# Kernel optimization log

Hardware: AMD Instinct MI355X
Metric: run time of the kernel (lower is better)

The kernel has to match this reference:

```python
import jax, jax.numpy as jnp
import numpy as np


def setup_inputs() -> dict:
    key = jax.random.key(0)
    k1, k2, k3 = jax.random.split(key, 3)
    N, C_in, H, W = 16, 64, 256, 256
    C_out, K = 128, 3
    x = jax.random.normal(k1, (N, C_in, H, W), dtype=jnp.float32)
    # kaiming-ish small init for stability through tanh
    conv_weight = jax.random.normal(k2, (C_out, C_in, K, K), dtype=jnp.float32) * 0.05
    conv_bias = jax.random.normal(k3, (C_out,), dtype=jnp.float32) * 0.05
    return {"x": x, "conv_weight": conv_weight, "conv_bias": conv_bias}


def reference(x, conv_weight, conv_bias):
    # VALID conv, stride 1, NCHW / OIHW (matches the CUDA kernel: H_out = H - K + 1)
    y = jax.lax.conv_general_dilated(
        x, conv_weight,
        window_strides=(1, 1), padding='VALID',
        dimension_numbers=('NCHW', 'OIHW', 'NCHW'))
    y = y + conv_bias[None, :, None, None]
    # fused pattern: double tanh then per-pixel min over output channels (keepdim)
    y = jnp.tanh(jnp.tanh(y))
    out = jnp.min(y, axis=1, keepdims=True)  # (N, 1, H_out, W_out)
    return out
```

## Files before the change

kernel.cpp:

```cpp
#include <hip/hip_runtime.h>
#include <stdint.h>

typedef _Float16 half8 __attribute__((ext_vector_type(8)));
typedef float float4v __attribute__((ext_vector_type(4)));

#define H_IN 256
#define W_IN 256
#define H_OUT 254
#define W_OUT 254
#define T_COLS 68
#define A_ROWS 408
#define A_BYTES (A_ROWS * 128)
#define B_SLAB  8192
#define B_BYTES (3 * B_SLAB)
#define MIN_BYTES (2 * 256 * 4)
#define SMEM_BYTES (A_BYTES + B_BYTES + MIN_BYTES)

__global__ void pack_w_kernel(const float* __restrict__ w, _Float16* __restrict__ Bp3) {
    int idx = blockIdx.x * 256 + threadIdx.x;
    if (idx >= 73728) return;
    int g   = idx >> 12;
    int rem = idx & 4095;
    int co  = rem >> 5;
    int s16 = (rem >> 3) & 3;
    int e   = rem & 7;
    int q   = s16 ^ ((co >> 2) & 3);
    int tap = g >> 1, h = g & 1;
    int cin = h * 32 + q * 8 + e;
    int kh  = tap / 3, kw = tap - kh * 3;
    Bp3[idx] = (_Float16)w[(co * 64 + cin) * 9 + kh * 3 + kw];
}

__device__ __forceinline__ int akey(int row) {
    return (((row & 7) ^ ((row >> 3) & 7)) << 4);
}

__global__ __launch_bounds__(512, 4)
void conv_v8_kernel(const float* __restrict__ x,
                    const _Float16* __restrict__ Bp3,
                    const float* __restrict__ bias,
                    float* __restrict__ out) {
    extern __shared__ __align__(16) char smem[];
    char*  Alds   = smem;
    char*  Blds   = smem + A_BYTES;
    float* minbuf = (float*)(smem + A_BYTES + B_BYTES);

    const int tid  = threadIdx.x;
    const int lane = tid & 63;
    const int wave = tid >> 6;
    const int ow0  = blockIdx.x * 64;
    const int oh0  = blockIdx.y * 4;
    const int nb   = blockIdx.z;
    const int wr   = wave >> 1;
    const int wc   = wave & 1;
    const int q    = lane >> 4;
    const int lr   = lane & 15;

#pragma unroll
    for (int s = 0; s < 2; ++s) {
        const char* src = (const char*)Bp3 + s * B_SLAB + tid * 16;
        char* dstb = Blds + s * B_SLAB + (tid & ~63) * 16;
        __builtin_amdgcn_global_load_lds(
            (const __attribute__((address_space(1))) uint32_t*)src,
            (__attribute__((address_space(3))) uint32_t*)dstb, 16, 0, 0);
    }

    float bv[4];
#pragma unroll
    for (int n = 0; n < 4; ++n) bv[n] = bias[wc * 64 + n * 16 + lr];

    {
        const float* xb = x + (size_t)nb * (64 * H_IN * W_IN);
#pragma unroll
        for (int k = 0; k < 2; ++k) {
            int id = tid + 512 * k;
            if (id < 816) {
                int oct  = (unsigned)id / 102u;
                int pxq  = id - oct * 102;
                int row0 = pxq * 4;
                int r    = (unsigned)row0 / (unsigned)T_COLS;
                int c    = row0 - r * T_COLS;
                int ih   = oh0 + r; if (ih > H_IN - 1) ih = H_IN - 1;
                int iw   = ow0 + c; if (iw > W_IN - 4) iw = W_IN - 4;
                const float* src = xb + (size_t)(oct * 8) * (H_IN * W_IN)
                                      + (size_t)ih * W_IN + iw;
                float4v f[8];
#pragma unroll
                for (int u = 0; u < 8; ++u)
                    f[u] = *(const float4v*)(src + (size_t)u * (H_IN * W_IN));
#pragma unroll
                for (int j = 0; j < 4; ++j) {
                    int row = row0 + j;
                    half8 hv;
#pragma unroll
                    for (int u = 0; u < 8; ++u) hv[u] = (_Float16)f[u][j];
                    *(half8*)(Alds + row * 128 + ((oct * 16) ^ akey(row))) = hv;
                }
            }
        }
    }
    __syncthreads();

    float4v acc[4][4];
#pragma unroll
    for (int m = 0; m < 4; ++m)
#pragma unroll
        for (int n = 0; n < 4; ++n)
#pragma unroll
            for (int i = 0; i < 4; ++i) acc[m][n][i] = 0.0f;

    const int bslot = (q ^ ((lr >> 2) & 3)) << 4;
    const int bco   = (wc * 64 + lr) * 64;

#pragma unroll
    for (int g = 0; g < 18; ++g) {
        if (g < 17) asm volatile("s_waitcnt vmcnt(1)" ::: "memory");
        else        asm volatile("s_waitcnt vmcnt(0)" ::: "memory");
        __builtin_amdgcn_s_barrier();
        __builtin_amdgcn_sched_barrier(0);

        if (g < 16) {
            const char* src = (const char*)Bp3 + (size_t)(g + 2) * B_SLAB + tid * 16;
            char* dstb = Blds + ((g + 2) % 3) * B_SLAB + (tid & ~63) * 16;
            __builtin_amdgcn_global_load_lds(
                (const __attribute__((address_space(1))) uint32_t*)src,
                (__attribute__((address_space(3))) uint32_t*)dstb, 16, 0, 0);
        }

        const int tap = g >> 1, h = g & 1;
        const int kh = tap / 3, kw = tap - kh * 3;
        const int kb = h * 64 + q * 16;

        half8 a[4], b[4];
#pragma unroll
        for (int n = 0; n < 4; ++n)
            b[n] = *(const half8*)(Blds + (g % 3) * B_SLAB + bco + n * 1024 + bslot);
#pragma unroll
        for (int m = 0; m < 4; ++m) {
            int row = (wr + kh) * T_COLS + m * 16 + lr + kw;
            a[m] = *(const half8*)(Alds + row * 128 + (kb ^ akey(row)));
        }

        __builtin_amdgcn_s_setprio(1);
#pragma unroll
        for (int m = 0; m < 4; ++m)
#pragma unroll
            for (int n = 0; n < 4; ++n)
                acc[m][n] = __builtin_amdgcn_mfma_f32_16x16x32_f16(
                    a[m], b[n], acc[m][n], 0, 0, 0);
        __builtin_amdgcn_s_setprio(0);
    }

#pragma unroll
    for (int m = 0; m < 4; ++m) {
        float4v v;
#pragma unroll
        for (int n = 0; n < 4; ++n) {
#pragma unroll
            for (int i = 0; i < 4; ++i) {
                float t = acc[m][n][i] + bv[n];
                v[i] = (n == 0) ? t : fminf(v[i], t);
            }
        }
#pragma unroll
        for (int off = 1; off < 16; off <<= 1)
#pragma unroll
            for (int i = 0; i < 4; ++i)
                v[i] = fminf(v[i], __shfl_xor(v[i], off, 64));
        if (lr == 0) {
#pragma unroll
            for (int i = 0; i < 4; ++i)
                minbuf[wc * 256 + wr * 64 + m * 16 + q * 4 + i] = v[i];
        }
    }
    __syncthreads();

    if (tid < 256) {
        int r = tid >> 6, c = tid & 63;
        int oh = oh0 + r, ow = ow0 + c;
        if (oh < H_OUT && ow < W_OUT) {
            float mv = fminf(minbuf[tid], minbuf[256 + tid]);
            out[((size_t)nb * H_OUT + oh) * W_OUT + ow] = tanhf(tanhf(mv));
        }
    }
}

extern "C" void kernel_launch(void* const* d_in, const int* in_sizes, int n_in,
                              void* d_out, int out_size, void* d_ws, size_t ws_size,
                              hipStream_t stream) {
    const float* x    = (const float*)d_in[0];
    const float* w    = (const float*)d_in[1];
    const float* bias = (const float*)d_in[2];
    float* out        = (float*)d_out;
    _Float16* Bp3     = (_Float16*)d_ws;

    pack_w_kernel<<<dim3(288), dim3(256), 0, stream>>>(w, Bp3);
    conv_v8_kernel<<<dim3(4, 64, 16), dim3(512), SMEM_BYTES, stream>>>(x, Bp3, bias, out);
}
```

Before: 168.6 us.

## Halve block to 4 waves with 8x4 MFMA tiles and register double-buffered LDS fragments

Each block now runs 256 threads (4 waves) instead of 512, and each wave computes 8x4 MFMA tiles covering two output rows. A and B fragments are prefetched from LDS into registers one k-step ahead, and B slabs are loaded three ahead with two loads per thread. The aim is more MFMA work per LDS fragment load and overlap of LDS reads with compute. The cost is a much larger accumulator register footprint (128 floats plus double-buffered fragments), which limits occupancy. The input staging loop also takes more iterations per thread.

```diff
diff --git a/kernel.cpp b/kernel.cpp
--- a/kernel.cpp
+++ b/kernel.cpp
@@ -35,8 +35,8 @@
     return (((row & 7) ^ ((row >> 3) & 7)) << 4);
 }
 
-__global__ __launch_bounds__(512, 4)
-void conv_v8_kernel(const float* __restrict__ x,
+__global__ __launch_bounds__(256, 2)
+void conv_v9_kernel(const float* __restrict__ x,
                     const _Float16* __restrict__ Bp3,
                     const float* __restrict__ bias,
                     float* __restrict__ out) {
@@ -57,102 +57,120 @@
     const int lr   = lane & 15;
 
 #pragma unroll
-    for (int s = 0; s < 2; ++s) {
-        const char* src = (const char*)Bp3 + s * B_SLAB + tid * 16;
-        char* dstb = Blds + s * B_SLAB + (tid & ~63) * 16;
-        __builtin_amdgcn_global_load_lds(
-            (const __attribute__((address_space(1))) uint32_t*)src,
-            (__attribute__((address_space(3))) uint32_t*)dstb, 16, 0, 0);
-    }
-
-    float bv[4];
-#pragma unroll
-    for (int n = 0; n < 4; ++n) bv[n] = bias[wc * 64 + n * 16 + lr];
-
-    {
-        const float* xb = x + (size_t)nb * (64 * H_IN * W_IN);
-#pragma unroll
-        for (int k = 0; k < 2; ++k) {
-            int id = tid + 512 * k;
-            if (id < 816) {
-                int oct  = (unsigned)id / 102u;
-                int pxq  = id - oct * 102;
-                int row0 = pxq * 4;
-                int r    = (unsigned)row0 / (unsigned)T_COLS;
-                int c    = row0 - r * T_COLS;
-                int ih   = oh0 + r; if (ih > H_IN - 1) ih = H_IN - 1;
-                int iw   = ow0 + c; if (iw > W_IN - 4) iw = W_IN - 4;
-                const float* src = xb + (size_t)(oct * 8) * (H_IN * W_IN)
-                                      + (size_t)ih * W_IN + iw;
-                float4v f[8];
-#pragma unroll
-                for (int u = 0; u < 8; ++u)
-                    f[u] = *(const float4v*)(src + (size_t)u * (H_IN * W_IN));
-#pragma unroll
-                for (int j = 0; j < 4; ++j) {
-                    int row = row0 + j;
-                    half8 hv;
-#pragma unroll
-                    for (int u = 0; u < 8; ++u) hv[u] = (_Float16)f[u][j];
-                    *(half8*)(Alds + row * 128 + ((oct * 16) ^ akey(row))) = hv;
-                }
-            }
-        }
-    }
-    __syncthreads();
-
-    float4v acc[4][4];
-#pragma unroll
-    for (int m = 0; m < 4; ++m)
-#pragma unroll
-        for (int n = 0; n < 4; ++n)
-#pragma unroll
-            for (int i = 0; i < 4; ++i) acc[m][n][i] = 0.0f;
-
-    const int bslot = (q ^ ((lr >> 2) & 3)) << 4;
-    const int bco   = (wc * 64 + lr) * 64;
-
-#pragma unroll
-    for (int g = 0; g < 18; ++g) {
-        if (g < 17) asm volatile("s_waitcnt vmcnt(1)" ::: "memory");
-        else        asm volatile("s_waitcnt vmcnt(0)" ::: "memory");
-        __builtin_amdgcn_s_barrier();
-        __builtin_amdgcn_sched_barrier(0);
-
-        if (g < 16) {
-            const char* src = (const char*)Bp3 + (size_t)(g + 2) * B_SLAB + tid * 16;
-            char* dstb = Blds + ((g + 2) % 3) * B_SLAB + (tid & ~63) * 16;
+    for (int s = 0; s < 3; ++s) {
+#pragma unroll
+        for (int i = 0; i < 2; ++i) {
+            const char* src = (const char*)Bp3 + s * B_SLAB + i * 4096 + tid * 16;
+            char* dstb = Blds + s * B_SLAB + i * 4096 + (tid & ~63) * 16;
             __builtin_amdgcn_global_load_lds(
                 (const __attribute__((address_space(1))) uint32_t*)src,
                 (__attribute__((address_space(3))) uint32_t*)dstb, 16, 0, 0);
         }
-
-        const int tap = g >> 1, h = g & 1;
+    }
+
+    float bv[4];
+#pragma unroll
+    for (int n = 0; n < 4; ++n) bv[n] = bias[wc * 64 + n * 16 + lr];
+
+    {
+        const float* xb = x + (size_t)nb * (64 * H_IN * W_IN);
+        for (int id = tid; id < 816; id += 256) {
+            int oct  = (unsigned)id / 102u;
+            int pxq  = id - oct * 102;
+            int row0 = pxq * 4;
+            int r    = (unsigned)row0 / (unsigned)T_COLS;
+            int c    = row0 - r * T_COLS;
+            int ih   = oh0 + r; if (ih > H_IN - 1) ih = H_IN - 1;
+            int iw   = ow0 + c; if (iw > W_IN - 4) iw = W_IN - 4;
+            const float* src = xb + (size_t)(oct * 8) * (H_IN * W_IN)
+                                  + (size_t)ih * W_IN + iw;
+            float4v f[8];
+#pragma unroll
+            for (int u = 0; u < 8; ++u)
+                f[u] = *(const float4v*)(src + (size_t)u * (H_IN * W_IN));
+#pragma unroll
+            for (int j = 0; j < 4; ++j) {
+                int row = row0 + j;
+                half8 hv;
+#pragma unroll
+                for (int u = 0; u < 8; ++u) hv[u] = (_Float16)f[u][j];
+                *(half8*)(Alds + row * 128 + ((oct * 16) ^ akey(row))) = hv;
+            }
+        }
+    }
+    __syncthreads();
+
+    const int bslot = (q ^ ((lr >> 2) & 3)) << 4;
+    const int bco   = (wc * 64 + lr) * 64;
+
+    float4v acc[8][4];
+#pragma unroll
+    for (int m = 0; m < 8; ++m)
+#pragma unroll
+        for (int n = 0; n < 4; ++n)
+#pragma unroll
+            for (int i = 0; i < 4; ++i) acc[m][n][i] = 0.0f;
+
+    half8 acur[8], bcur[4], anxt[8], bnxt[4];
+
+    auto loadA = [&](int gg, half8 (&dst)[8]) {
+        const int tap = gg >> 1, hh = gg & 1;
         const int kh = tap / 3, kw = tap - kh * 3;
-        const int kb = h * 64 + q * 16;
-
-        half8 a[4], b[4];
+        const int kb = hh * 64 + q * 16;
+#pragma unroll
+        for (int m = 0; m < 8; ++m) {
+            int row = (wr * 2 + (m >> 2) + kh) * T_COLS + (m & 3) * 16 + lr + kw;
+            dst[m] = *(const half8*)(Alds + row * 128 + (kb ^ akey(row)));
+        }
+    };
+    auto loadB = [&](int gg, half8 (&dst)[4]) {
 #pragma unroll
         for (int n = 0; n < 4; ++n)
-            b[n] = *(const half8*)(Blds + (g % 3) * B_SLAB + bco + n * 1024 + bslot);
-#pragma unroll
-        for (int m = 0; m < 4; ++m) {
-            int row = (wr + kh) * T_COLS + m * 16 + lr + kw;
-            a[m] = *(const half8*)(Alds + row * 128 + (kb ^ akey(row)));
-        }
-
+            dst[n] = *(const half8*)(Blds + (gg % 3) * B_SLAB + bco + n * 1024 + bslot);
+    };
+
+    loadA(0, acur);
+    loadB(0, bcur);
+
+#pragma unroll
+    for (int g = 0; g < 18; ++g) {
+        if (g < 16)      asm volatile("s_waitcnt vmcnt(2)" ::: "memory");
+        else if (g == 16) asm volatile("s_waitcnt vmcnt(0)" ::: "memory");
+        if (g < 17) __builtin_amdgcn_s_barrier();
+
+        if (g < 15) {
+#pragma unroll
+            for (int i = 0; i < 2; ++i) {
+                const char* src = (const char*)Bp3 + (size_t)(g + 3) * B_SLAB
+                                  + i * 4096 + tid * 16;
+                char* dstb = Blds + ((g + 3) % 3) * B_SLAB + i * 4096
+                                  + (tid & ~63) * 16;
+                __builtin_amdgcn_global_load_lds(
+                    (const __attribute__((address_space(1))) uint32_t*)src,
+                    (__attribute__((address_space(3))) uint32_t*)dstb, 16, 0, 0);
+            }
+        }
+
+        if (g < 17) {
+            if (g & 1) { loadA(g + 1, acur); loadB(g + 1, bcur); }
+            else       { loadA(g + 1, anxt); loadB(g + 1, bnxt); }
+            __builtin_amdgcn_sched_group_barrier(0x100, 12, 0);
+        }
+
+        half8 (&A)[8] = (g & 1) ? anxt : acur;
+        half8 (&B)[4] = (g & 1) ? bnxt : bcur;
         __builtin_amdgcn_s_setprio(1);
 #pragma unroll
-        for (int m = 0; m < 4; ++m)
+        for (int m = 0; m < 8; ++m)
 #pragma unroll
             for (int n = 0; n < 4; ++n)
                 acc[m][n] = __builtin_amdgcn_mfma_f32_16x16x32_f16(
-                    a[m], b[n], acc[m][n], 0, 0, 0);
+                    A[m], B[n], acc[m][n], 0, 0, 0);
         __builtin_amdgcn_s_setprio(0);
     }
 
 #pragma unroll
-    for (int m = 0; m < 4; ++m) {
+    for (int m = 0; m < 8; ++m) {
         float4v v;
 #pragma unroll
         for (int n = 0; n < 4; ++n) {
@@ -170,12 +188,12 @@
         if (lr == 0) {
 #pragma unroll
             for (int i = 0; i < 4; ++i)
-                minbuf[wc * 256 + wr * 64 + m * 16 + q * 4 + i] = v[i];
+                minbuf[wc * 256 + wr * 128 + m * 16 + q * 4 + i] = v[i];
         }
     }
     __syncthreads();
 
-    if (tid < 256) {
+    {
         int r = tid >> 6, c = tid & 63;
         int oh = oh0 + r, ow = ow0 + c;
         if (oh < H_OUT && ow < W_OUT) {
@@ -195,5 +213,5 @@
     _Float16* Bp3     = (_Float16*)d_ws;
 
     pack_w_kernel<<<dim3(288), dim3(256), 0, stream>>>(w, Bp3);
-    conv_v8_kernel<<<dim3(4, 64, 16), dim3(512), SMEM_BYTES, stream>>>(x, Bp3, bias, out);
-}
+    conv_v9_kernel<<<dim3(4, 64, 16), dim3(256), SMEM_BYTES, stream>>>(x, Bp3, bias, out);
+}
```

After: 253.4 us. 50.3% more time.

## Deepen weight ring to four slabs and register-double-buffer LDS fragments

Applied to the files above, without the earlier changes.

The weight staging ring in LDS grows from three to four slabs, with a prefetch distance of three, so weights are fetched further ahead of use. The A and B fragments for the next K-step are now read from LDS into a second register set while the current step's MFMAs run, with sched_group_barrier hints to interleave the LDS reads and MFMAs. The goal is to hide LDS read latency and global-to-LDS latency behind matrix math. The cost is more LDS per block and more registers, and launch bounds drop from 4 to 2 blocks per CU, which may reduce occupancy.

```diff
diff --git a/kernel.cpp b/kernel.cpp
--- a/kernel.cpp
+++ b/kernel.cpp
@@ -12,7 +12,7 @@
 #define A_ROWS 408
 #define A_BYTES (A_ROWS * 128)
 #define B_SLAB  8192
-#define B_BYTES (3 * B_SLAB)
+#define B_BYTES (4 * B_SLAB)
 #define MIN_BYTES (2 * 256 * 4)
 #define SMEM_BYTES (A_BYTES + B_BYTES + MIN_BYTES)
 
@@ -35,11 +35,11 @@
     return (((row & 7) ^ ((row >> 3) & 7)) << 4);
 }
 
-__global__ __launch_bounds__(512, 4)
-void conv_v8_kernel(const float* __restrict__ x,
-                    const _Float16* __restrict__ Bp3,
-                    const float* __restrict__ bias,
-                    float* __restrict__ out) {
+__global__ __launch_bounds__(512, 2)
+void conv_v10_kernel(const float* __restrict__ x,
+                     const _Float16* __restrict__ Bp3,
+                     const float* __restrict__ bias,
+                     float* __restrict__ out) {
     extern __shared__ __align__(16) char smem[];
     char*  Alds   = smem;
     char*  Blds   = smem + A_BYTES;
@@ -57,7 +57,7 @@
     const int lr   = lane & 15;
 
 #pragma unroll
-    for (int s = 0; s < 2; ++s) {
+    for (int s = 0; s < 3; ++s) {
         const char* src = (const char*)Bp3 + s * B_SLAB + tid * 16;
         char* dstb = Blds + s * B_SLAB + (tid & ~63) * 16;
         __builtin_amdgcn_global_load_lds(
@@ -101,54 +101,70 @@
     }
     __syncthreads();
 
-    float4v acc[4][4];
-#pragma unroll
-    for (int m = 0; m < 4; ++m)
-#pragma unroll
-        for (int n = 0; n < 4; ++n)
-#pragma unroll
-            for (int i = 0; i < 4; ++i) acc[m][n][i] = 0.0f;
-
     const int bslot = (q ^ ((lr >> 2) & 3)) << 4;
     const int bco   = (wc * 64 + lr) * 64;
 
+    float4v acc[4][4];
+#pragma unroll
+    for (int m = 0; m < 4; ++m)
+#pragma unroll
+        for (int n = 0; n < 4; ++n)
+#pragma unroll
+            for (int i = 0; i < 4; ++i) acc[m][n][i] = 0.0f;
+
+    half8 acur[4], bcur[4], anxt[4], bnxt[4];
+
+    auto loadA = [&](int gg, half8 (&dst)[4]) {
+        const int tap = gg >> 1, hh = gg & 1;
+        const int kh = tap / 3, kw = tap - kh * 3;
+        const int kb = hh * 64 + q * 16;
+#pragma unroll
+        for (int m = 0; m < 4; ++m) {
+            int row = (wr + kh) * T_COLS + m * 16 + lr + kw;
+            dst[m] = *(const half8*)(Alds + row * 128 + (kb ^ akey(row)));
+        }
+    };
+    auto loadB = [&](int gg, half8 (&dst)[4]) {
+#pragma unroll
+        for (int n = 0; n < 4; ++n)
+            dst[n] = *(const half8*)(Blds + (gg & 3) * B_SLAB + bco + n * 1024 + bslot);
+    };
+
+    loadA(0, acur);
+    loadB(0, bcur);
+
 #pragma unroll
     for (int g = 0; g < 18; ++g) {
-        if (g < 17) asm volatile("s_waitcnt vmcnt(1)" ::: "memory");
-        else        asm volatile("s_waitcnt vmcnt(0)" ::: "memory");
-        __builtin_amdgcn_s_barrier();
-        __builtin_amdgcn_sched_barrier(0);
-
-        if (g < 16) {
-            const char* src = (const char*)Bp3 + (size_t)(g + 2) * B_SLAB + tid * 16;
-            char* dstb = Blds + ((g + 2) % 3) * B_SLAB + (tid & ~63) * 16;
+        if (g < 16)       asm volatile("s_waitcnt vmcnt(1)" ::: "memory");
+        else if (g == 16) asm volatile("s_waitcnt vmcnt(0)" ::: "memory");
+        if (g < 16) __builtin_amdgcn_s_barrier();
+
+        if (g < 15) {
+            const char* src = (const char*)Bp3 + (size_t)(g + 3) * B_SLAB + tid * 16;
+            char* dstb = Blds + ((g + 3) & 3) * B_SLAB + (tid & ~63) * 16;
             __builtin_amdgcn_global_load_lds(
                 (const __attribute__((address_space(1))) uint32_t*)src,
                 (__attribute__((address_space(3))) uint32_t*)dstb, 16, 0, 0);
         }
 
-        const int tap = g >> 1, h = g & 1;
-        const int kh = tap / 3, kw = tap - kh * 3;
-        const int kb = h * 64 + q * 16;
-
-        half8 a[4], b[4];
-#pragma unroll
-        for (int n = 0; n < 4; ++n)
-            b[n] = *(const half8*)(Blds + (g % 3) * B_SLAB + bco + n * 1024 + bslot);
-#pragma unroll
-        for (int m = 0; m < 4; ++m) {
-            int row = (wr + kh) * T_COLS + m * 16 + lr + kw;
-            a[m] = *(const half8*)(Alds + row * 128 + (kb ^ akey(row)));
-        }
-
+        if (g < 17) {
+            if (g & 1) { loadA(g + 1, acur); loadB(g + 1, bcur); }
+            else       { loadA(g + 1, anxt); loadB(g + 1, bnxt); }
+        }
+
+        half8 (&A)[4] = (g & 1) ? anxt : acur;
+        half8 (&B)[4] = (g & 1) ? bnxt : bcur;
+
+        __builtin_amdgcn_sched_group_barrier(0x100, 8, 0);
         __builtin_amdgcn_s_setprio(1);
 #pragma unroll
         for (int m = 0; m < 4; ++m)
 #pragma unroll
             for (int n = 0; n < 4; ++n)
                 acc[m][n] = __builtin_amdgcn_mfma_f32_16x16x32_f16(
-                    a[m], b[n], acc[m][n], 0, 0, 0);
+                    A[m], B[n], acc[m][n], 0, 0, 0);
         __builtin_amdgcn_s_setprio(0);
+        __builtin_amdgcn_sched_group_barrier(0x8, 16, 0);
     }
 
 #pragma unroll
@@ -195,5 +211,5 @@
     _Float16* Bp3     = (_Float16*)d_ws;
 
     pack_w_kernel<<<dim3(288), dim3(256), 0, stream>>>(w, Bp3);
-    conv_v8_kernel<<<dim3(4, 64, 16), dim3(512), SMEM_BYTES, stream>>>(x, Bp3, bias, out);
-}
+    conv_v10_kernel<<<dim3(4, 64, 16), dim3(512), SMEM_BYTES, stream>>>(x, Bp3, bias, out);
+}
```

After: 226.5 us. 1.34x slower.

## Make blocks loop over row strips with double-buffered input tiles and per-tap weight slabs

Applied to the files above, without the earlier changes.

Each block now walks 16 consecutive 4-row output tiles of a 64-row strip instead of one tile. The next tile's input is prefetched into registers during the current tile's MMA loop and written into a second LDS buffer. Weights are repacked into one 16KB slab per tap and streamed with double buffering. This amortizes launch and prologue cost and overlaps input loading with compute. In exchange it uses much more LDS, lowering occupancy to about one block per CU, and leaves a small 256-block grid.

```diff
diff --git a/kernel.cpp b/kernel.cpp
--- a/kernel.cpp
+++ b/kernel.cpp
@@ -11,177 +11,205 @@
 #define T_COLS 68
 #define A_ROWS 408
 #define A_BYTES (A_ROWS * 128)
-#define B_SLAB  8192
-#define B_BYTES (3 * B_SLAB)
-#define MIN_BYTES (2 * 256 * 4)
-#define SMEM_BYTES (A_BYTES + B_BYTES + MIN_BYTES)
-
-__global__ void pack_w_kernel(const float* __restrict__ w, _Float16* __restrict__ Bp3) {
+#define B_SLAB  16384
+#define SMEM_BYTES (2*A_BYTES + 2*B_SLAB + 2048)
+
+__global__ void pack_w_kernel(const float* __restrict__ w, _Float16* __restrict__ Bp) {
     int idx = blockIdx.x * 256 + threadIdx.x;
     if (idx >= 73728) return;
-    int g   = idx >> 12;
-    int rem = idx & 4095;
-    int co  = rem >> 5;
-    int s16 = (rem >> 3) & 3;
+    int tap = idx >> 13;
+    int rem = idx & 8191;
+    int co  = rem >> 6;
+    int s   = (rem >> 3) & 7;
     int e   = rem & 7;
-    int q   = s16 ^ ((co >> 2) & 3);
-    int tap = g >> 1, h = g & 1;
+    int hq  = s ^ (co & 7);
+    int h   = hq >> 2, q = hq & 3;
     int cin = h * 32 + q * 8 + e;
     int kh  = tap / 3, kw = tap - kh * 3;
-    Bp3[idx] = (_Float16)w[(co * 64 + cin) * 9 + kh * 3 + kw];
+    Bp[idx] = (_Float16)w[(co * 64 + cin) * 9 + kh * 3 + kw];
 }
 
 __device__ __forceinline__ int akey(int row) {
     return (((row & 7) ^ ((row >> 3) & 7)) << 4);
 }
 
-__global__ __launch_bounds__(512, 4)
-void conv_v8_kernel(const float* __restrict__ x,
-                    const _Float16* __restrict__ Bp3,
-                    const float* __restrict__ bias,
-                    float* __restrict__ out) {
+__global__ __launch_bounds__(512, 2)
+void conv_v11_kernel(const float* __restrict__ x,
+                     const _Float16* __restrict__ Bp,
+                     const float* __restrict__ bias,
+                     float* __restrict__ out) {
     extern __shared__ __align__(16) char smem[];
-    char*  Alds   = smem;
-    char*  Blds   = smem + A_BYTES;
-    float* minbuf = (float*)(smem + A_BYTES + B_BYTES);
+    char*  AldsBase = smem;
+    char*  Blds     = smem + 2 * A_BYTES;
+    float* minbuf   = (float*)(smem + 2 * A_BYTES + 2 * B_SLAB);
 
     const int tid  = threadIdx.x;
     const int lane = tid & 63;
     const int wave = tid >> 6;
     const int ow0  = blockIdx.x * 64;
-    const int oh0  = blockIdx.y * 4;
+    const int strip0 = blockIdx.y * 64;
     const int nb   = blockIdx.z;
     const int wr   = wave >> 1;
     const int wc   = wave & 1;
     const int q    = lane >> 4;
     const int lr   = lane & 15;
 
-#pragma unroll
-    for (int s = 0; s < 2; ++s) {
-        const char* src = (const char*)Bp3 + s * B_SLAB + tid * 16;
-        char* dstb = Blds + s * B_SLAB + (tid & ~63) * 16;
-        __builtin_amdgcn_global_load_lds(
-            (const __attribute__((address_space(1))) uint32_t*)src,
-            (__attribute__((address_space(3))) uint32_t*)dstb, 16, 0, 0);
+    const float* xb = x + (size_t)nb * (64 * H_IN * W_IN);
+
+    int id0 = tid;
+    int id1 = (tid < 304) ? (512 + tid) : tid;
+    const bool w1 = (tid < 304);
+    int  s_oct[2], s_row0[2], s_r[2], s_iw[2];
+    {
+        int ids[2] = {id0, id1};
+#pragma unroll
+        for (int k = 0; k < 2; ++k) {
+            int o   = (unsigned)ids[k] / 102u;
+            int pxq = ids[k] - o * 102;
+            int r   = (unsigned)pxq / 17u;
+            int c4  = (pxq - r * 17) * 4;
+            s_oct[k] = o; s_row0[k] = pxq * 4; s_r[k] = r;
+            int iw = ow0 + c4; if (iw > W_IN - 4) iw = W_IN - 4;
+            s_iw[k] = iw;
+        }
     }
-
-    float bv[4];
-#pragma unroll
-    for (int n = 0; n < 4; ++n) bv[n] = bias[wc * 64 + n * 16 + lr];
-
-    {
-        const float* xb = x + (size_t)nb * (64 * H_IN * W_IN);
+    float4v f[2][8];
+
+    auto issue_loads = [&](int ih0) {
 #pragma unroll
         for (int k = 0; k < 2; ++k) {
-            int id = tid + 512 * k;
-            if (id < 816) {
-                int oct  = (unsigned)id / 102u;
-                int pxq  = id - oct * 102;
-                int row0 = pxq * 4;
-                int r    = (unsigned)row0 / (unsigned)T_COLS;
-                int c    = row0 - r * T_COLS;
-                int ih   = oh0 + r; if (ih > H_IN - 1) ih = H_IN - 1;
-                int iw   = ow0 + c; if (iw > W_IN - 4) iw = W_IN - 4;
-                const float* src = xb + (size_t)(oct * 8) * (H_IN * W_IN)
-                                      + (size_t)ih * W_IN + iw;
-                float4v f[8];
-#pragma unroll
-                for (int u = 0; u < 8; ++u)
-                    f[u] = *(const float4v*)(src + (size_t)u * (H_IN * W_IN));
-#pragma unroll
-                for (int j = 0; j < 4; ++j) {
-                    int row = row0 + j;
-                    half8 hv;
-#pragma unroll
-                    for (int u = 0; u < 8; ++u) hv[u] = (_Float16)f[u][j];
-                    *(half8*)(Alds + row * 128 + ((oct * 16) ^ akey(row))) = hv;
-                }
-            }
-        }
-    }
-    __syncthreads();
-
-    float4v acc[4][4];
-#pragma unroll
-    for (int m = 0; m < 4; ++m)
-#pragma unroll
-        for (int n = 0; n < 4; ++n)
-#pragma unroll
-            for (int i = 0; i < 4; ++i) acc[m][n][i] = 0.0f;
-
-    const int bslot = (q ^ ((lr >> 2) & 3)) << 4;
-    const int bco   = (wc * 64 + lr) * 64;
-
-#pragma unroll
-    for (int g = 0; g < 18; ++g) {
-        if (g < 17) asm volatile("s_waitcnt vmcnt(1)" ::: "memory");
-        else        asm volatile("s_waitcnt vmcnt(0)" ::: "memory");
-        __builtin_amdgcn_s_barrier();
-        __builtin_amdgcn_sched_barrier(0);
-
-        if (g < 16) {
-            const char* src = (const char*)Bp3 + (size_t)(g + 2) * B_SLAB + tid * 16;
-            char* dstb = Blds + ((g + 2) % 3) * B_SLAB + (tid & ~63) * 16;
+            int ih = ih0 + s_r[k]; if (ih > H_IN - 1) ih = H_IN - 1;
+            const float* src = xb + (size_t)(s_oct[k] * 8) * (H_IN * W_IN)
+                                  + (size_t)ih * W_IN + s_iw[k];
+#pragma unroll
+            for (int u = 0; u < 8; ++u)
+                f[k][u] = *(const float4v*)(src + (size_t)u * (H_IN * W_IN));
+        }
+    };
+    auto write_A = [&](char* abuf) {
+#pragma unroll
+        for (int k = 0; k < 2; ++k) {
+            if (k == 1 && !w1) continue;
+#pragma unroll
+            for (int j = 0; j < 4; ++j) {
+                int row = s_row0[k] + j;
+                half8 hv;
+#pragma unroll
+                for (int u = 0; u < 8; ++u) hv[u] = (_Float16)f[k][u][j];
+                *(half8*)(abuf + row * 128 + ((s_oct[k] * 16) ^ akey(row))) = hv;
+            }
+        }
+    };
+    auto dma_slab = [&](int srctap, int slot) {
+#pragma unroll
+        for (int i = 0; i < 2; ++i) {
+            const char* src = (const char*)Bp + (size_t)srctap * B_SLAB + i * 8192 + tid * 16;
+            char* dst = Blds + slot * B_SLAB + i * 8192 + (tid & ~63) * 16;
             __builtin_amdgcn_global_load_lds(
                 (const __attribute__((address_space(1))) uint32_t*)src,
-                (__attribute__((address_space(3))) uint32_t*)dstb, 16, 0, 0);
-        }
-
-        const int tap = g >> 1, h = g & 1;
-        const int kh = tap / 3, kw = tap - kh * 3;
-        const int kb = h * 64 + q * 16;
-
-        half8 a[4], b[4];
-#pragma unroll
-        for (int n = 0; n < 4; ++n)
-            b[n] = *(const half8*)(Blds + (g % 3) * B_SLAB + bco + n * 1024 + bslot);
+                (__attribute__((address_space(3))) uint32_t*)dst, 16, 0, 0);
+        }
+    };
+
+    float bv[4];
+#pragma unroll
+    for (int n = 0; n < 4; ++n) bv[n] = bias[wc * 64 + n * 16 + lr];
+
+    dma_slab(0, 0);
+    __builtin_amdgcn_sched_barrier(0);
+    issue_loads(strip0);
+    write_A(AldsBase);
+
+    const int bco = (wc * 64 + lr) * 128;
+    const int bkey = ((wc * 64 + lr) & 7);
+
+    for (int t = 0; t < 16; ++t) {
+        char* abuf = AldsBase + (t & 1) * A_BYTES;
+        const int oh0 = strip0 + t * 4;
+
+        float4v acc[4][4];
+#pragma unroll
+        for (int m = 0; m < 4; ++m)
+#pragma unroll
+            for (int n = 0; n < 4; ++n)
+#pragma unroll
+                for (int i = 0; i < 4; ++i) acc[m][n][i] = 0.0f;
+
+#pragma unroll
+        for (int g = 0; g < 9; ++g) {
+            if (g == 8) asm volatile("s_waitcnt vmcnt(16) lgkmcnt(0)" ::: "memory");
+            else        asm volatile("s_waitcnt vmcnt(0) lgkmcnt(0)" ::: "memory");
+            __builtin_amdgcn_s_barrier();
+
+            dma_slab((g + 1 == 9) ? 0 : (g + 1), (t + g + 1) & 1);
+            __builtin_amdgcn_sched_barrier(0);
+            if (g == 7) {
+                issue_loads(oh0 + 4);
+                __builtin_amdgcn_sched_barrier(0);
+            }
+
+            const int kh = g / 3, kw = g - kh * 3;
+            const char* slab = Blds + ((t + g) & 1) * B_SLAB;
+
+            __builtin_amdgcn_s_setprio(1);
+#pragma unroll
+            for (int h = 0; h < 2; ++h) {
+                const int kb = h * 64 + q * 16;
+                half8 a[4], b[4];
+#pragma unroll
+                for (int n = 0; n < 4; ++n)
+                    b[n] = *(const half8*)(slab + bco + n * 2048
+                                           + (((h * 4 + q) ^ bkey) << 4));
+#pragma unroll
+                for (int m = 0; m < 4; ++m) {
+                    int row = (wr + kh) * T_COLS + m * 16 + lr + kw;
+                    a[m] = *(const half8*)(abuf + row * 128 + (kb ^ akey(row)));
+                }
+#pragma unroll
+                for (int m = 0; m < 4; ++m)
+#pragma unroll
+                    for (int n = 0; n < 4; ++n)
+                        acc[m][n] = __builtin_amdgcn_mfma_f32_16x16x32_f16(
+                            a[m], b[n], acc[m][n], 0, 0, 0);
+            }
+            __builtin_amdgcn_s_setprio(0);
+        }
+
 #pragma unroll
         for (int m = 0; m < 4; ++m) {
-            int row = (wr + kh) * T_COLS + m * 16 + lr + kw;
-            a[m] = *(const half8*)(Alds + row * 128 + (kb ^ akey(row)));
-        }
-
-        __builtin_amdgcn_s_setprio(1);
-#pragma unroll
-        for (int m = 0; m < 4; ++m)
-#pragma unroll
-            for (int n = 0; n < 4; ++n)
-                acc[m][n] = __builtin_amdgcn_mfma_f32_16x16x32_f16(
-                    a[m], b[n], acc[m][n], 0, 0, 0);
-        __builtin_amdgcn_s_setprio(0);
-    }
-
-#pragma unroll
-    for (int m = 0; m < 4; ++m) {
-        float4v v;
-#pragma unroll
-        for (int n = 0; n < 4; ++n) {
-#pragma unroll
-            for (int i = 0; i < 4; ++i) {
-                float t = acc[m][n][i] + bv[n];
-                v[i] = (n == 0) ? t : fminf(v[i], t);
-            }
-        }
-#pragma unroll
-        for (int off = 1; off < 16; off <<= 1)
-#pragma unroll
-            for (int i = 0; i < 4; ++i)
-                v[i] = fminf(v[i], __shfl_xor(v[i], off, 64));
-        if (lr == 0) {
-#pragma unroll
-            for (int i = 0; i < 4; ++i)
-                minbuf[wc * 256 + wr * 64 + m * 16 + q * 4 + i] = v[i];
-        }
-    }
-    __syncthreads();
-
-    if (tid < 256) {
-        int r = tid >> 6, c = tid & 63;
-        int oh = oh0 + r, ow = ow0 + c;
-        if (oh < H_OUT && ow < W_OUT) {
-            float mv = fminf(minbuf[tid], minbuf[256 + tid]);
-            out[((size_t)nb * H_OUT + oh) * W_OUT + ow] = tanhf(tanhf(mv));
-        }
+            float4v v;
+#pragma unroll
+            for (int n = 0; n < 4; ++n) {
+#pragma unroll
+                for (int i = 0; i < 4; ++i) {
+                    float tt = acc[m][n][i] + bv[n];
+                    v[i] = (n == 0) ? tt : fminf(v[i], tt);
+                }
+            }
+#pragma unroll
+            for (int off = 1; off < 16; off <<= 1)
+#pragma unroll
+                for (int i = 0; i < 4; ++i)
+                    v[i] = fminf(v[i], __shfl_xor(v[i], off, 64));
+            if (lr == 0) {
+#pragma unroll
+                for (int i = 0; i < 4; ++i)
+                    minbuf[wc * 256 + wr * 64 + m * 16 + q * 4 + i] = v[i];
+            }
+        }
+        asm volatile("s_waitcnt lgkmcnt(0)" ::: "memory");
+        __builtin_amdgcn_s_barrier();
+
+        if (tid < 256) {
+            int r = tid >> 6, c = tid & 63;
+            int oh = oh0 + r, ow = ow0 + c;
+            if (oh < H_OUT && ow < W_OUT) {
+                float mv = fminf(minbuf[tid], minbuf[256 + tid]);
+                out[((size_t)nb * H_OUT + oh) * W_OUT + ow] = tanhf(tanhf(mv));
+            }
+        }
+
+        write_A(AldsBase + ((t + 1) & 1) * A_BYTES);
     }
 }
 
@@ -192,8 +220,15 @@
     const float* w    = (const float*)d_in[1];
     const float* bias = (const float*)d_in[2];
     float* out        = (float*)d_out;
-    _Float16* Bp3     = (_Float16*)d_ws;
-
-    pack_w_kernel<<<dim3(288), dim3(256), 0, stream>>>(w, Bp3);
-    conv_v8_kernel<<<dim3(4, 64, 16), dim3(512), SMEM_BYTES, stream>>>(x, Bp3, bias, out);
-}
+    _Float16* Bp      = (_Float16*)d_ws;
+
+    static bool attr_set = false;
+    if (!attr_set) {
+        hipFuncSetAttribute((const void*)conv_v11_kernel,
+                            hipFuncAttributeMaxDynamicSharedMemorySize, SMEM_BYTES);
+        attr_set = true;
+    }
+
+    pack_w_kernel<<<dim3(288), dim3(256), 0, stream>>>(w, Bp);
+    conv_v11_kernel<<<dim3(4, 4, 16), dim3(512), SMEM_BYTES, stream>>>(x, Bp, bias, out);
+}
```

Result: slower. 473.4 us (+180.7%).
